# Kernel tuning notes

Measured on AMD Instinct MI355X. Metric: run time of the kernel, lower is better.

Reference implementation:

```python
import jax, jax.numpy as jnp
import numpy as np

QUALITY = 75

Y_TABLE = np.array([
    [16, 11, 10, 16, 24, 40, 51, 61],
    [12, 12, 14, 19, 26, 58, 60, 55],
    [14, 13, 16, 24, 40, 57, 69, 56],
    [14, 17, 22, 29, 51, 87, 80, 62],
    [18, 22, 37, 56, 68, 109, 103, 77],
    [24, 35, 55, 64, 81, 104, 113, 92],
    [49, 64, 78, 87, 103, 121, 120, 101],
    [72, 92, 95, 98, 112, 100, 103, 99]], dtype=np.float32)

C_TABLE = np.array([
    [17, 18, 24, 47, 99, 99, 99, 99],
    [18, 21, 26, 66, 99, 99, 99, 99],
    [24, 26, 56, 99, 99, 99, 99, 99],
    [47, 66, 99, 99, 99, 99, 99, 99],
    [99, 99, 99, 99, 99, 99, 99, 99],
    [99, 99, 99, 99, 99, 99, 99, 99],
    [99, 99, 99, 99, 99, 99, 99, 99],
    [99, 99, 99, 99, 99, 99, 99, 99]], dtype=np.float32)

def _dct_mat():
    # Orthonormal 8-point DCT-II matrix D: coef = D @ block @ D.T
    xg = np.arange(8, dtype=np.float64)
    ug = np.arange(8, dtype=np.float64)
    D = 0.5 * np.cos((2.0 * xg[None, :] + 1.0) * ug[:, None] * np.pi / 16.0)
    D[0, :] *= 1.0 / np.sqrt(2.0)
    return jnp.asarray(D, dtype=jnp.float32)

D8 = _dct_mat()

def _blockify(ch):
    # [B,H,W] -> [B, H//8, W//8, 8, 8]
    B, H, W = ch.shape
    return ch.reshape(B, H // 8, 8, W // 8, 8).transpose(0, 1, 3, 2, 4)

def _deblockify(blk):
    # [B, hb, wb, 8, 8] -> [B, hb*8, wb*8]
    B, hb, wb, _, _ = blk.shape
    return blk.transpose(0, 1, 3, 2, 4).reshape(B, hb * 8, wb * 8)

def _channel_jpeg(ch, table, factor):
    # ch: [B,H,W] in 0..255 -> quantize/dequantize in DCT domain
    q = table * factor  # [8,8]
    blk = _blockify(ch - 128.0)                                   # [B,hb,wb,8,8]
    coef = jnp.einsum('bhwxy,ux,vy->bhwuv', blk, D8, D8)           # 8x8 DCT
    coef = jnp.round(coef / q) * q                                 # quantize + dequantize
    rec = jnp.einsum('bhwuv,ux,vy->bhwxy', coef, D8, D8) + 128.0   # IDCT
    return _deblockify(rec)

def jpeg_compress(img, quality):
    # img: [B,3,H,W] in [0,1]
    if quality < 50:
        factor = 5000.0 / quality
    else:
        factor = 200.0 - 2.0 * quality
    factor = factor / 100.0
    x = img * 255.0
    r, g, b = x[:, 0], x[:, 1], x[:, 2]
    y = 0.299 * r + 0.587 * g + 0.114 * b
    cb = -0.168736 * r - 0.331264 * g + 0.5 * b + 128.0
    cr = 0.5 * r - 0.418688 * g - 0.081312 * b + 128.0
    # 4:2:0 chroma subsampling via 2x2 average pooling
    B, H, W = cb.shape
    cb_s = cb.reshape(B, H // 2, 2, W // 2, 2).mean(axis=(2, 4))
    cr_s = cr.reshape(B, H // 2, 2, W // 2, 2).mean(axis=(2, 4))
    y_r = _channel_jpeg(y, jnp.asarray(Y_TABLE), factor)
    cb_r = _channel_jpeg(cb_s, jnp.asarray(C_TABLE), factor)
    cr_r = _channel_jpeg(cr_s, jnp.asarray(C_TABLE), factor)
    # nearest-neighbor chroma upsampling
    cb_u = jnp.repeat(jnp.repeat(cb_r, 2, axis=1), 2, axis=2)
    cr_u = jnp.repeat(jnp.repeat(cr_r, 2, axis=1), 2, axis=2)
    cbm = cb_u - 128.0
    crm = cr_u - 128.0
    r2 = y_r + 1.402 * crm
    g2 = y_r - 0.344136 * cbm - 0.714136 * crm
    b2 = y_r + 1.772 * cbm
    out = jnp.stack([r2, g2, b2], axis=1)
    return jnp.clip(out, 0.0, 255.0) / 255.0


def setup_inputs() -> dict:
    key = jax.random.key(0)
    x = jax.random.uniform(key, (16, 3, 512, 512), dtype=jnp.float32)
    return {"x": x}


def reference(x):
    img_clip = jnp.clip(x, 0.0, 1.0)
    img_jpeg = jpeg_compress(img_clip, QUALITY)
    img_gap = jax.lax.stop_gradient(img_jpeg - x)
    return x + img_gap
```

## Files before the change

### kernel.cpp

```cpp
#include <hip/hip_runtime.h>
#include <math.h>

#define CH_STRIDE (512 * 512)

static constexpr float DMc[8][8] = {
  { 0.35355339059327373f, 0.35355339059327373f, 0.35355339059327373f, 0.35355339059327373f,
    0.35355339059327373f, 0.35355339059327373f, 0.35355339059327373f, 0.35355339059327373f},
  { 0.49039264020161522f, 0.41573480615127262f, 0.27778511650980111f, 0.09754516100806413f,
   -0.09754516100806413f,-0.27778511650980111f,-0.41573480615127262f,-0.49039264020161522f},
  { 0.46193976625564337f, 0.19134171618254489f,-0.19134171618254489f,-0.46193976625564337f,
   -0.46193976625564337f,-0.19134171618254489f, 0.19134171618254489f, 0.46193976625564337f},
  { 0.41573480615127262f,-0.09754516100806413f,-0.49039264020161522f,-0.27778511650980111f,
    0.27778511650980111f, 0.49039264020161522f, 0.09754516100806413f,-0.41573480615127262f},
  { 0.35355339059327373f,-0.35355339059327373f,-0.35355339059327373f, 0.35355339059327373f,
    0.35355339059327373f,-0.35355339059327373f,-0.35355339059327373f, 0.35355339059327373f},
  { 0.27778511650980111f,-0.49039264020161522f, 0.09754516100806413f, 0.41573480615127262f,
   -0.41573480615127262f,-0.09754516100806413f, 0.49039264020161522f,-0.27778511650980111f},
  { 0.19134171618254489f,-0.46193976625564337f, 0.46193976625564337f,-0.19134171618254489f,
   -0.19134171618254489f, 0.46193976625564337f,-0.46193976625564337f, 0.19134171618254489f},
  { 0.09754516100806413f,-0.27778511650980111f, 0.41573480615127262f,-0.49039264020161522f,
    0.49039264020161522f,-0.41573480615127262f, 0.27778511650980111f,-0.09754516100806413f},
};

static constexpr float QTABc[128] = {
   8.0f,  5.5f,  5.0f,  8.0f, 12.0f, 20.0f, 25.5f, 30.5f,
   6.0f,  6.0f,  7.0f,  9.5f, 13.0f, 29.0f, 30.0f, 27.5f,
   7.0f,  6.5f,  8.0f, 12.0f, 20.0f, 28.5f, 34.5f, 28.0f,
   7.0f,  8.5f, 11.0f, 14.5f, 25.5f, 43.5f, 40.0f, 31.0f,
   9.0f, 11.0f, 18.5f, 28.0f, 34.0f, 54.5f, 51.5f, 38.5f,
  12.0f, 17.5f, 27.5f, 32.0f, 40.5f, 52.0f, 56.5f, 46.0f,
  24.5f, 32.0f, 39.0f, 43.5f, 51.5f, 60.5f, 60.0f, 50.5f,
  36.0f, 46.0f, 47.5f, 49.0f, 56.0f, 50.0f, 51.5f, 49.5f,

   8.5f,  9.0f, 12.0f, 23.5f, 49.5f, 49.5f, 49.5f, 49.5f,
   9.0f, 10.5f, 13.0f, 33.0f, 49.5f, 49.5f, 49.5f, 49.5f,
  12.0f, 13.0f, 28.0f, 49.5f, 49.5f, 49.5f, 49.5f, 49.5f,
  23.5f, 33.0f, 49.5f, 49.5f, 49.5f, 49.5f, 49.5f, 49.5f,
  49.5f, 49.5f, 49.5f, 49.5f, 49.5f, 49.5f, 49.5f, 49.5f,
  49.5f, 49.5f, 49.5f, 49.5f, 49.5f, 49.5f, 49.5f, 49.5f,
  49.5f, 49.5f, 49.5f, 49.5f, 49.5f, 49.5f, 49.5f, 49.5f,
  49.5f, 49.5f, 49.5f, 49.5f, 49.5f, 49.5f, 49.5f, 49.5f,
};

__device__ __forceinline__ float fm(float a, float b) { return __fmul_rn(a, b); }
__device__ __forceinline__ float fa(float a, float b) { return __fadd_rn(a, b); }
__device__ __forceinline__ float fs(float a, float b) { return __fsub_rn(a, b); }
__device__ __forceinline__ float fd(float a, float b) { return __fdiv_rn(a, b); }

__global__ __launch_bounds__(192, 4)
void jpeg_kernel(const float* __restrict__ x, float* __restrict__ out) {
  const int tid = threadIdx.x;
  const int q  = blockIdx.x;
  const int b  = q >> 8;
  const int qq = q & 255;
  const int row0 = (qq >> 4) << 5;
  const int col0 = (qq & 15) << 5;

  __shared__ __align__(16) float Ys[32][36];
  __shared__ __align__(16) float Cb[16][20];
  __shared__ __align__(16) float Cr[16][20];
  __shared__ __align__(16) float Cq[24][8][9];

  auto stage1 = [&](int qd) {
    const int pr = qd >> 3;
    const int pc = (qd & 7) << 2;
    const size_t ib = ((((size_t)b * 3) * 512 + (size_t)(row0 + pr)) * 512) + (size_t)(col0 + pc);
    float4 rv = *(const float4*)(x + ib);
    float4 gv = *(const float4*)(x + ib + CH_STRIDE);
    float4 bv = *(const float4*)(x + ib + 2 * CH_STRIDE);
    float xr[4] = {rv.x, rv.y, rv.z, rv.w};
    float xg[4] = {gv.x, gv.y, gv.z, gv.w};
    float xb[4] = {bv.x, bv.y, bv.z, bv.w};
    float yo[4], cbv[4], crv[4];
#pragma unroll
    for (int i = 0; i < 4; ++i) {
      float r  = fm(fminf(fmaxf(xr[i], 0.0f), 1.0f), 255.0f);
      float g  = fm(fminf(fmaxf(xg[i], 0.0f), 1.0f), 255.0f);
      float bb = fm(fminf(fmaxf(xb[i], 0.0f), 1.0f), 255.0f);
      float y  = fa(fa(fm(0.299f, r), fm(0.587f, g)), fm(0.114f, bb));
      yo[i]  = fs(y, 128.0f);
      cbv[i] = fa(fa(fs(fm(-0.168736f, r), fm(0.331264f, g)), fm(0.5f, bb)), 128.0f);
      crv[i] = fa(fs(fs(fm(0.5f, r), fm(0.418688f, g)), fm(0.081312f, bb)), 128.0f);
    }
    *(float4*)&Ys[pr][pc] = make_float4(yo[0], yo[1], yo[2], yo[3]);

    float cbh0 = fa(cbv[0], cbv[1]), cbh1 = fa(cbv[2], cbv[3]);
    float crh0 = fa(crv[0], crv[1]), crh1 = fa(crv[2], crv[3]);
    float pcb0 = __shfl_xor(cbh0, 8, 64);
    float pcb1 = __shfl_xor(cbh1, 8, 64);
    float pcr0 = __shfl_xor(crh0, 8, 64);
    float pcr1 = __shfl_xor(crh1, 8, 64);
    if (((qd >> 3) & 1) == 0) {
      const int ii = pr >> 1, jc = pc >> 1;
      Cb[ii][jc]     = fs(fm(fa(cbh0, pcb0), 0.25f), 128.0f);
      Cb[ii][jc + 1] = fs(fm(fa(cbh1, pcb1), 0.25f), 128.0f);
      Cr[ii][jc]     = fs(fm(fa(crh0, pcr0), 0.25f), 128.0f);
      Cr[ii][jc + 1] = fs(fm(fa(crh1, pcr1), 0.25f), 128.0f);
    }
  };
  stage1(tid);
  if (tid < 64) stage1(192 + tid);
  __syncthreads();

  const int  blk = tid >> 3;
  const int  j   = tid & 7;
  const bool isY = blk < 16;
  const float* src;
  float*       wdst;
  int ld;
  const float* qr = QTABc + j * 8;
  if (isY) {
    const int by = blk >> 2, bx = blk & 3;
    src = &Ys[by * 8][bx * 8];  wdst = &Ys[by * 8 + j][bx * 8];  ld = 36;
  } else if (blk < 20) {
    const int c = blk - 16, cy = c >> 1, cx = c & 1;
    src = &Cb[cy * 8][cx * 8];  wdst = &Cb[cy * 8 + j][cx * 8];  ld = 20;  qr += 64;
  } else {
    const int c = blk - 20, cy = c >> 1, cx = c & 1;
    src = &Cr[cy * 8][cx * 8];  wdst = &Cr[cy * 8 + j][cx * 8];  ld = 20;  qr += 64;
  }

  {
    float dj[8];
#pragma unroll
    for (int xx = 0; xx < 8; ++xx) dj[xx] = DMc[j][xx];
    float s[8][4];
#pragma unroll
    for (int v = 0; v < 8; ++v) { s[v][0] = 0.0f; s[v][1] = 0.0f; s[v][2] = 0.0f; s[v][3] = 0.0f; }
    const float* srow = src;
#pragma unroll
    for (int xx = 0; xx < 8; ++xx) {
      float4 aq = *(const float4*)(srow);
      float4 bq = *(const float4*)(srow + 4);
      srow += ld;
      float t0r[8] = { fm(aq.x, dj[xx]), fm(aq.y, dj[xx]), fm(aq.z, dj[xx]), fm(aq.w, dj[xx]),
                       fm(bq.x, dj[xx]), fm(bq.y, dj[xx]), fm(bq.z, dj[xx]), fm(bq.w, dj[xx]) };
#pragma unroll
      for (int v = 0; v < 8; ++v) {
        s[v][0] = fa(s[v][0], fm(t0r[0], DMc[v][0]));
        s[v][1] = fa(s[v][1], fm(t0r[1], DMc[v][1]));
        s[v][2] = fa(s[v][2], fm(t0r[2], DMc[v][2]));
        s[v][3] = fa(s[v][3], fm(t0r[3], DMc[v][3]));
        s[v][0] = fa(s[v][0], fm(t0r[4], DMc[v][4]));
        s[v][1] = fa(s[v][1], fm(t0r[5], DMc[v][5]));
        s[v][2] = fa(s[v][2], fm(t0r[6], DMc[v][6]));
        s[v][3] = fa(s[v][3], fm(t0r[7], DMc[v][7]));
      }
    }
    float* cq = &Cq[blk][j][0];
#pragma unroll
    for (int v = 0; v < 8; ++v) {
      float coef = fa(fa(s[v][0], s[v][1]), fa(s[v][2], s[v][3]));
      float qv = qr[v];
      cq[v] = fm(rintf(fd(coef, qv)), qv);
    }
  }

  asm volatile("s_waitcnt lgkmcnt(0)" ::: "memory");

  {
    float acc[8];
#pragma unroll
    for (int yy = 0; yy < 8; ++yy) acc[yy] = 0.0f;
    const float* cqb = &Cq[blk][0][0];
#pragma unroll
    for (int u = 0; u < 8; ++u) {
      float du = DMc[u][j];
      float t2r[8];
#pragma unroll
      for (int v = 0; v < 8; ++v) t2r[v] = fm(cqb[u * 9 + v], du);
#pragma unroll
      for (int yy = 0; yy < 8; ++yy) {
#pragma unroll
        for (int v = 0; v < 8; ++v)
          acc[yy] = fa(acc[yy], fm(t2r[v], DMc[v][yy]));
      }
    }
    float r0[8];
#pragma unroll
    for (int yy = 0; yy < 8; ++yy) {
      float rec = fa(acc[yy], 128.0f);
      r0[yy] = isY ? rec : fs(rec, 128.0f);
    }
    *(float4*)(wdst)     = make_float4(r0[0], r0[1], r0[2], r0[3]);
    *(float4*)(wdst + 4) = make_float4(r0[4], r0[5], r0[6], r0[7]);
  }
  __syncthreads();

  auto stage5 = [&](int qd) {
    const int pr = qd >> 3;
    const int pc = (qd & 7) << 2;
    const size_t ib = ((((size_t)b * 3) * 512 + (size_t)(row0 + pr)) * 512) + (size_t)(col0 + pc);
    float4 rv = *(const float4*)(x + ib);
    float4 gv = *(const float4*)(x + ib + CH_STRIDE);
    float4 bv = *(const float4*)(x + ib + 2 * CH_STRIDE);
    float xr[4] = {rv.x, rv.y, rv.z, rv.w};
    float xg[4] = {gv.x, gv.y, gv.z, gv.w};
    float xb[4] = {bv.x, bv.y, bv.z, bv.w};
    float ro[4], go[4], bo[4];
    const int hr = pr >> 1;
#pragma unroll
    for (int i = 0; i < 4; ++i) {
      float y_r = Ys[pr][pc + i];
      float cbm = Cb[hr][(pc + i) >> 1];
      float crm = Cr[hr][(pc + i) >> 1];
      float r2 = fa(y_r, fm(1.402f, crm));
      float g2 = fs(fs(y_r, fm(0.344136f, cbm)), fm(0.714136f, crm));
      float b2 = fa(y_r, fm(1.772f, cbm));
      float jr = fd(fminf(fmaxf(r2, 0.0f), 255.0f), 255.0f);
      float jg = fd(fminf(fmaxf(g2, 0.0f), 255.0f), 255.0f);
      float jb = fd(fminf(fmaxf(b2, 0.0f), 255.0f), 255.0f);
      ro[i] = fa(xr[i], fs(jr, xr[i]));
      go[i] = fa(xg[i], fs(jg, xg[i]));
      bo[i] = fa(xb[i], fs(jb, xb[i]));
    }
    *(float4*)(out + ib)                 = make_float4(ro[0], ro[1], ro[2], ro[3]);
    *(float4*)(out + ib + CH_STRIDE)     = make_float4(go[0], go[1], go[2], go[3]);
    *(float4*)(out + ib + 2 * CH_STRIDE) = make_float4(bo[0], bo[1], bo[2], bo[3]);
  };
  stage5(tid);
  if (tid < 64) stage5(192 + tid);
}

extern "C" void kernel_launch(void* const* d_in, const int* in_sizes, int n_in,
                              void* d_out, int out_size, void* d_ws, size_t ws_size,
                              hipStream_t stream) {
  const float* x = (const float*)d_in[0];
  float* out = (float*)d_out;
  jpeg_kernel<<<dim3(4096), dim3(192), 0, stream>>>(x, out);
}
```

Baseline: 116.6 us.

## Process two tiles per block and spread extra pixel quads across all waves

Each block now loops over two 32x32 tiles, and the launch grid is halved to match. The 64 leftover pixel quads per tile are spread across all three waves (16/16/32 lanes) instead of all going to wave 0, which balances the stage-1 and stage-5 work. The DCT inputs and quantized coefficients are loaded from LDS into register arrays up front, with Cq padded to 10 floats and read as float2. This trades per-block launch overhead and wave imbalance for higher register pressure and an extra barrier between the two tiles.

Result: slower. 155.8 us (+33.6%).

```diff
diff --git a/kernel.cpp b/kernel.cpp
--- a/kernel.cpp
+++ b/kernel.cpp
@@ -49,58 +49,18 @@
 
 __global__ __launch_bounds__(192, 4)
 void jpeg_kernel(const float* __restrict__ x, float* __restrict__ out) {
-  const int tid = threadIdx.x;
-  const int q  = blockIdx.x;
-  const int b  = q >> 8;
-  const int qq = q & 255;
-  const int row0 = (qq >> 4) << 5;
-  const int col0 = (qq & 15) << 5;
+  const int tid  = threadIdx.x;
+  const int lane = tid & 63;
+  const int wav  = tid >> 6;
 
   __shared__ __align__(16) float Ys[32][36];
   __shared__ __align__(16) float Cb[16][20];
   __shared__ __align__(16) float Cr[16][20];
-  __shared__ __align__(16) float Cq[24][8][9];
-
-  auto stage1 = [&](int qd) {
-    const int pr = qd >> 3;
-    const int pc = (qd & 7) << 2;
-    const size_t ib = ((((size_t)b * 3) * 512 + (size_t)(row0 + pr)) * 512) + (size_t)(col0 + pc);
-    float4 rv = *(const float4*)(x + ib);
-    float4 gv = *(const float4*)(x + ib + CH_STRIDE);
-    float4 bv = *(const float4*)(x + ib + 2 * CH_STRIDE);
-    float xr[4] = {rv.x, rv.y, rv.z, rv.w};
-    float xg[4] = {gv.x, gv.y, gv.z, gv.w};
-    float xb[4] = {bv.x, bv.y, bv.z, bv.w};
-    float yo[4], cbv[4], crv[4];
-#pragma unroll
-    for (int i = 0; i < 4; ++i) {
-      float r  = fm(fminf(fmaxf(xr[i], 0.0f), 1.0f), 255.0f);
-      float g  = fm(fminf(fmaxf(xg[i], 0.0f), 1.0f), 255.0f);
-      float bb = fm(fminf(fmaxf(xb[i], 0.0f), 1.0f), 255.0f);
-      float y  = fa(fa(fm(0.299f, r), fm(0.587f, g)), fm(0.114f, bb));
-      yo[i]  = fs(y, 128.0f);
-      cbv[i] = fa(fa(fs(fm(-0.168736f, r), fm(0.331264f, g)), fm(0.5f, bb)), 128.0f);
-      crv[i] = fa(fs(fs(fm(0.5f, r), fm(0.418688f, g)), fm(0.081312f, bb)), 128.0f);
-    }
-    *(float4*)&Ys[pr][pc] = make_float4(yo[0], yo[1], yo[2], yo[3]);
-
-    float cbh0 = fa(cbv[0], cbv[1]), cbh1 = fa(cbv[2], cbv[3]);
-    float crh0 = fa(crv[0], crv[1]), crh1 = fa(crv[2], crv[3]);
-    float pcb0 = __shfl_xor(cbh0, 8, 64);
-    float pcb1 = __shfl_xor(cbh1, 8, 64);
-    float pcr0 = __shfl_xor(crh0, 8, 64);
-    float pcr1 = __shfl_xor(crh1, 8, 64);
-    if (((qd >> 3) & 1) == 0) {
-      const int ii = pr >> 1, jc = pc >> 1;
-      Cb[ii][jc]     = fs(fm(fa(cbh0, pcb0), 0.25f), 128.0f);
-      Cb[ii][jc + 1] = fs(fm(fa(cbh1, pcb1), 0.25f), 128.0f);
-      Cr[ii][jc]     = fs(fm(fa(crh0, pcr0), 0.25f), 128.0f);
-      Cr[ii][jc + 1] = fs(fm(fa(crh1, pcr1), 0.25f), 128.0f);
-    }
-  };
-  stage1(tid);
-  if (tid < 64) stage1(192 + tid);
-  __syncthreads();
+  __shared__ __align__(16) float Cq[24][8][10];
+
+  const int eq = (wav == 0) ? (lane < 16 ? 192 + lane : -1)
+               : (wav == 1) ? (lane < 16 ? 208 + lane : -1)
+                            : (lane < 32 ? 224 + lane : -1);
 
   const int  blk = tid >> 3;
   const int  j   = tid & 7;
@@ -120,106 +80,185 @@
     src = &Cr[cy * 8][cx * 8];  wdst = &Cr[cy * 8 + j][cx * 8];  ld = 20;  qr += 64;
   }
 
-  {
-    float dj[8];
-#pragma unroll
-    for (int xx = 0; xx < 8; ++xx) dj[xx] = DMc[j][xx];
-    float s[8][4];
-#pragma unroll
-    for (int v = 0; v < 8; ++v) { s[v][0] = 0.0f; s[v][1] = 0.0f; s[v][2] = 0.0f; s[v][3] = 0.0f; }
-    const float* srow = src;
-#pragma unroll
-    for (int xx = 0; xx < 8; ++xx) {
-      float4 aq = *(const float4*)(srow);
-      float4 bq = *(const float4*)(srow + 4);
-      srow += ld;
-      float t0r[8] = { fm(aq.x, dj[xx]), fm(aq.y, dj[xx]), fm(aq.z, dj[xx]), fm(aq.w, dj[xx]),
-                       fm(bq.x, dj[xx]), fm(bq.y, dj[xx]), fm(bq.z, dj[xx]), fm(bq.w, dj[xx]) };
+  for (int tt = 0; tt < 2; ++tt) {
+    const int tile = (blockIdx.x << 1) + tt;
+    const int b  = tile >> 8;
+    const int qq = tile & 255;
+    const int row0 = (qq >> 4) << 5;
+    const int col0 = (qq & 15) << 5;
+
+    auto stage1 = [&](int qd) {
+      const int pr = qd >> 3;
+      const int pc = (qd & 7) << 2;
+      const size_t ib = ((((size_t)b * 3) * 512 + (size_t)(row0 + pr)) * 512) + (size_t)(col0 + pc);
+      float4 rv = *(const float4*)(x + ib);
+      float4 gv = *(const float4*)(x + ib + CH_STRIDE);
+      float4 bv = *(const float4*)(x + ib + 2 * CH_STRIDE);
+      float xr[4] = {rv.x, rv.y, rv.z, rv.w};
+      float xg[4] = {gv.x, gv.y, gv.z, gv.w};
+      float xb[4] = {bv.x, bv.y, bv.z, bv.w};
+      float yo[4], cbv[4], crv[4];
+#pragma unroll
+      for (int i = 0; i < 4; ++i) {
+        float r  = fm(fminf(fmaxf(xr[i], 0.0f), 1.0f), 255.0f);
+        float g  = fm(fminf(fmaxf(xg[i], 0.0f), 1.0f), 255.0f);
+        float bb = fm(fminf(fmaxf(xb[i], 0.0f), 1.0f), 255.0f);
+        float y  = fa(fa(fm(0.299f, r), fm(0.587f, g)), fm(0.114f, bb));
+        yo[i]  = fs(y, 128.0f);
+        cbv[i] = fa(fa(fs(fm(-0.168736f, r), fm(0.331264f, g)), fm(0.5f, bb)), 128.0f);
+        crv[i] = fa(fs(fs(fm(0.5f, r), fm(0.418688f, g)), fm(0.081312f, bb)), 128.0f);
+      }
+      *(float4*)&Ys[pr][pc] = make_float4(yo[0], yo[1], yo[2], yo[3]);
+
+      float cbh0 = fa(cbv[0], cbv[1]), cbh1 = fa(cbv[2], cbv[3]);
+      float crh0 = fa(crv[0], crv[1]), crh1 = fa(crv[2], crv[3]);
+      float pcb0 = __shfl_xor(cbh0, 8, 64);
+      float pcb1 = __shfl_xor(cbh1, 8, 64);
+      float pcr0 = __shfl_xor(crh0, 8, 64);
+      float pcr1 = __shfl_xor(crh1, 8, 64);
+      if (((qd >> 3) & 1) == 0) {
+        const int ii = pr >> 1, jc = pc >> 1;
+        Cb[ii][jc]     = fs(fm(fa(cbh0, pcb0), 0.25f), 128.0f);
+        Cb[ii][jc + 1] = fs(fm(fa(cbh1, pcb1), 0.25f), 128.0f);
+        Cr[ii][jc]     = fs(fm(fa(crh0, pcr0), 0.25f), 128.0f);
+        Cr[ii][jc + 1] = fs(fm(fa(crh1, pcr1), 0.25f), 128.0f);
+      }
+    };
+    stage1(tid);
+    if (eq >= 0) stage1(eq);
+    __syncthreads();
+
+    {
+      float rd[64];
+      {
+        const float* srow = src;
+#pragma unroll
+        for (int xx = 0; xx < 8; ++xx) {
+          float4 aq = *(const float4*)(srow);
+          float4 bq = *(const float4*)(srow + 4);
+          srow += ld;
+          rd[xx * 8 + 0] = aq.x; rd[xx * 8 + 1] = aq.y; rd[xx * 8 + 2] = aq.z; rd[xx * 8 + 3] = aq.w;
+          rd[xx * 8 + 4] = bq.x; rd[xx * 8 + 5] = bq.y; rd[xx * 8 + 6] = bq.z; rd[xx * 8 + 7] = bq.w;
+        }
+      }
+      float dj[8];
+#pragma unroll
+      for (int xx = 0; xx < 8; ++xx) dj[xx] = DMc[j][xx];
+      float t0[64];
+#pragma unroll
+      for (int xx = 0; xx < 8; ++xx)
+#pragma unroll
+        for (int yy = 0; yy < 8; ++yy)
+          t0[xx * 8 + yy] = fm(rd[xx * 8 + yy], dj[xx]);
+
+      float s[8][4];
+#pragma unroll
+      for (int v = 0; v < 8; ++v) { s[v][0] = 0.0f; s[v][1] = 0.0f; s[v][2] = 0.0f; s[v][3] = 0.0f; }
+#pragma unroll
+      for (int xx = 0; xx < 8; ++xx) {
+        const int k = xx * 8;
+#pragma unroll
+        for (int v = 0; v < 8; ++v) {
+          s[v][0] = fa(s[v][0], fm(t0[k + 0], DMc[v][0]));
+          s[v][1] = fa(s[v][1], fm(t0[k + 1], DMc[v][1]));
+          s[v][2] = fa(s[v][2], fm(t0[k + 2], DMc[v][2]));
+          s[v][3] = fa(s[v][3], fm(t0[k + 3], DMc[v][3]));
+          s[v][0] = fa(s[v][0], fm(t0[k + 4], DMc[v][4]));
+          s[v][1] = fa(s[v][1], fm(t0[k + 5], DMc[v][5]));
+          s[v][2] = fa(s[v][2], fm(t0[k + 6], DMc[v][6]));
+          s[v][3] = fa(s[v][3], fm(t0[k + 7], DMc[v][7]));
+        }
+      }
+      float* cq = &Cq[blk][j][0];
 #pragma unroll
       for (int v = 0; v < 8; ++v) {
-        s[v][0] = fa(s[v][0], fm(t0r[0], DMc[v][0]));
-        s[v][1] = fa(s[v][1], fm(t0r[1], DMc[v][1]));
-        s[v][2] = fa(s[v][2], fm(t0r[2], DMc[v][2]));
-        s[v][3] = fa(s[v][3], fm(t0r[3], DMc[v][3]));
-        s[v][0] = fa(s[v][0], fm(t0r[4], DMc[v][4]));
-        s[v][1] = fa(s[v][1], fm(t0r[5], DMc[v][5]));
-        s[v][2] = fa(s[v][2], fm(t0r[6], DMc[v][6]));
-        s[v][3] = fa(s[v][3], fm(t0r[7], DMc[v][7]));
+        float coef = fa(fa(s[v][0], s[v][1]), fa(s[v][2], s[v][3]));
+        float qv = qr[v];
+        cq[v] = fm(rintf(fd(coef, qv)), qv);
       }
     }
-    float* cq = &Cq[blk][j][0];
-#pragma unroll
-    for (int v = 0; v < 8; ++v) {
-      float coef = fa(fa(s[v][0], s[v][1]), fa(s[v][2], s[v][3]));
-      float qv = qr[v];
-      cq[v] = fm(rintf(fd(coef, qv)), qv);
+
+    asm volatile("s_waitcnt lgkmcnt(0)" ::: "memory");
+
+    {
+      float tc[64];
+      {
+        const float* cqb = &Cq[blk][0][0];
+#pragma unroll
+        for (int u = 0; u < 8; ++u) {
+          float2 p0 = *(const float2*)(cqb + u * 10);
+          float2 p1 = *(const float2*)(cqb + u * 10 + 2);
+          float2 p2 = *(const float2*)(cqb + u * 10 + 4);
+          float2 p3 = *(const float2*)(cqb + u * 10 + 6);
+          tc[u * 8 + 0] = p0.x; tc[u * 8 + 1] = p0.y;
+          tc[u * 8 + 2] = p1.x; tc[u * 8 + 3] = p1.y;
+          tc[u * 8 + 4] = p2.x; tc[u * 8 + 5] = p2.y;
+          tc[u * 8 + 6] = p3.x; tc[u * 8 + 7] = p3.y;
+        }
+      }
+      float acc[8];
+#pragma unroll
+      for (int yy = 0; yy < 8; ++yy) acc[yy] = 0.0f;
+#pragma unroll
+      for (int u = 0; u < 8; ++u) {
+        float du = DMc[u][j];
+        float t2r[8];
+#pragma unroll
+        for (int v = 0; v < 8; ++v) t2r[v] = fm(tc[u * 8 + v], du);
+#pragma unroll
+        for (int yy = 0; yy < 8; ++yy) {
+#pragma unroll
+          for (int v = 0; v < 8; ++v)
+            acc[yy] = fa(acc[yy], fm(t2r[v], DMc[v][yy]));
+        }
+      }
+      float r0[8];
+#pragma unroll
+      for (int yy = 0; yy < 8; ++yy) {
+        float rec = fa(acc[yy], 128.0f);
+        r0[yy] = isY ? rec : fs(rec, 128.0f);
+      }
+      *(float4*)(wdst)     = make_float4(r0[0], r0[1], r0[2], r0[3]);
+      *(float4*)(wdst + 4) = make_float4(r0[4], r0[5], r0[6], r0[7]);
     }
+    __syncthreads();
+
+    auto stage5 = [&](int qd) {
+      const int pr = qd >> 3;
+      const int pc = (qd & 7) << 2;
+      const size_t ib = ((((size_t)b * 3) * 512 + (size_t)(row0 + pr)) * 512) + (size_t)(col0 + pc);
+      float4 rv = *(const float4*)(x + ib);
+      float4 gv = *(const float4*)(x + ib + CH_STRIDE);
+      float4 bv = *(const float4*)(x + ib + 2 * CH_STRIDE);
+      float xr[4] = {rv.x, rv.y, rv.z, rv.w};
+      float xg[4] = {gv.x, gv.y, gv.z, gv.w};
+      float xb[4] = {bv.x, bv.y, bv.z, bv.w};
+      float ro[4], go[4], bo[4];
+      const int hr = pr >> 1;
+#pragma unroll
+      for (int i = 0; i < 4; ++i) {
+        float y_r = Ys[pr][pc + i];
+        float cbm = Cb[hr][(pc + i) >> 1];
+        float crm = Cr[hr][(pc + i) >> 1];
+        float r2 = fa(y_r, fm(1.402f, crm));
+        float g2 = fs(fs(y_r, fm(0.344136f, cbm)), fm(0.714136f, crm));
+        float b2 = fa(y_r, fm(1.772f, cbm));
+        float jr = fd(fminf(fmaxf(r2, 0.0f), 255.0f), 255.0f);
+        float jg = fd(fminf(fmaxf(g2, 0.0f), 255.0f), 255.0f);
+        float jb = fd(fminf(fmaxf(b2, 0.0f), 255.0f), 255.0f);
+        ro[i] = fa(xr[i], fs(jr, xr[i]));
+        go[i] = fa(xg[i], fs(jg, xg[i]));
+        bo[i] = fa(xb[i], fs(jb, xb[i]));
+      }
+      *(float4*)(out + ib)                 = make_float4(ro[0], ro[1], ro[2], ro[3]);
+      *(float4*)(out + ib + CH_STRIDE)     = make_float4(go[0], go[1], go[2], go[3]);
+      *(float4*)(out + ib + 2 * CH_STRIDE) = make_float4(bo[0], bo[1], bo[2], bo[3]);
+    };
+    stage5(tid);
+    if (eq >= 0) stage5(eq);
+
+    if (tt == 0) __syncthreads();
   }
-
-  asm volatile("s_waitcnt lgkmcnt(0)" ::: "memory");
-
-  {
-    float acc[8];
-#pragma unroll
-    for (int yy = 0; yy < 8; ++yy) acc[yy] = 0.0f;
-    const float* cqb = &Cq[blk][0][0];
-#pragma unroll
-    for (int u = 0; u < 8; ++u) {
-      float du = DMc[u][j];
-      float t2r[8];
-#pragma unroll
-      for (int v = 0; v < 8; ++v) t2r[v] = fm(cqb[u * 9 + v], du);
-#pragma unroll
-      for (int yy = 0; yy < 8; ++yy) {
-#pragma unroll
-        for (int v = 0; v < 8; ++v)
-          acc[yy] = fa(acc[yy], fm(t2r[v], DMc[v][yy]));
-      }
-    }
-    float r0[8];
-#pragma unroll
-    for (int yy = 0; yy < 8; ++yy) {
-      float rec = fa(acc[yy], 128.0f);
-      r0[yy] = isY ? rec : fs(rec, 128.0f);
-    }
-    *(float4*)(wdst)     = make_float4(r0[0], r0[1], r0[2], r0[3]);
-    *(float4*)(wdst + 4) = make_float4(r0[4], r0[5], r0[6], r0[7]);
-  }
-  __syncthreads();
-
-  auto stage5 = [&](int qd) {
-    const int pr = qd >> 3;
-    const int pc = (qd & 7) << 2;
-    const size_t ib = ((((size_t)b * 3) * 512 + (size_t)(row0 + pr)) * 512) + (size_t)(col0 + pc);
-    float4 rv = *(const float4*)(x + ib);
-    float4 gv = *(const float4*)(x + ib + CH_STRIDE);
-    float4 bv = *(const float4*)(x + ib + 2 * CH_STRIDE);
-    float xr[4] = {rv.x, rv.y, rv.z, rv.w};
-    float xg[4] = {gv.x, gv.y, gv.z, gv.w};
-    float xb[4] = {bv.x, bv.y, bv.z, bv.w};
-    float ro[4], go[4], bo[4];
-    const int hr = pr >> 1;
-#pragma unroll
-    for (int i = 0; i < 4; ++i) {
-      float y_r = Ys[pr][pc + i];
-      float cbm = Cb[hr][(pc + i) >> 1];
-      float crm = Cr[hr][(pc + i) >> 1];
-      float r2 = fa(y_r, fm(1.402f, crm));
-      float g2 = fs(fs(y_r, fm(0.344136f, cbm)), fm(0.714136f, crm));
-      float b2 = fa(y_r, fm(1.772f, cbm));
-      float jr = fd(fminf(fmaxf(r2, 0.0f), 255.0f), 255.0f);
-      float jg = fd(fminf(fmaxf(g2, 0.0f), 255.0f), 255.0f);
-      float jb = fd(fminf(fmaxf(b2, 0.0f), 255.0f), 255.0f);
-      ro[i] = fa(xr[i], fs(jr, xr[i]));
-      go[i] = fa(xg[i], fs(jg, xg[i]));
-      bo[i] = fa(xb[i], fs(jb, xb[i]));
-    }
-    *(float4*)(out + ib)                 = make_float4(ro[0], ro[1], ro[2], ro[3]);
-    *(float4*)(out + ib + CH_STRIDE)     = make_float4(go[0], go[1], go[2], go[3]);
-    *(float4*)(out + ib + 2 * CH_STRIDE) = make_float4(bo[0], bo[1], bo[2], bo[3]);
-  };
-  stage5(tid);
-  if (tid < 64) stage5(192 + tid);
 }
 
 extern "C" void kernel_launch(void* const* d_in, const int* in_sizes, int n_in,
@@ -227,5 +266,5 @@
                               hipStream_t stream) {
   const float* x = (const float*)d_in[0];
   float* out = (float*)d_out;
-  jpeg_kernel<<<dim3(4096), dim3(192), 0, stream>>>(x, out);
+  jpeg_kernel<<<dim3(2048), dim3(192), 0, stream>>>(x, out);
 }
```
